# Kernel optimization log

Measured on AMD Instinct MI355X. Metric: run time of the kernel, lower is better.

The kernel has to match this reference:

```python
import jax, jax.numpy as jnp
import numpy as np

# Model constants (match init_kwargs)
NUM_HEADS = 8
IN_BITS = 64
N_STATE = 256
N_OUT = 64
K_CONN = 8            # n_bits_per_output_neuron
HASH = 65536          # hash_size
K_BITS = 3            # routing key bits
B = 128               # batch of independent sequences
T = 128               # timesteps (windows) per sequence


def setup_inputs() -> dict:
    key = jax.random.key(0)
    k1, k2, k3, k4, k5, k6 = jax.random.split(key, 6)
    # flat bit sequences, split into T windows of IN_BITS in reference()
    bits = jax.random.randint(k1, (B, T * IN_BITS), 0, 2, dtype=jnp.int32)
    # state layer: full connectivity (default n_bits_per_state_neuron =
    # input_bits + n_state_neurons), hashed addressing via random odd-ish
    # integer coefficients dotted with the bit vector, mod HASH.
    total_in = IN_BITS + N_STATE  # 320
    state_coeffs = jax.random.randint(k2, (N_STATE, total_in), 1, HASH, dtype=jnp.int32)
    state_mem = jax.random.uniform(k3, (N_STATE, HASH), dtype=jnp.float32)
    # output heads: each neuron connects to K_CONN random state bits
    head_conn = jax.random.randint(k4, (NUM_HEADS, N_OUT, K_CONN), 0, N_STATE, dtype=jnp.int32)
    head_coeffs = jax.random.randint(k5, (NUM_HEADS, N_OUT, K_CONN), 1, HASH, dtype=jnp.int32)
    head_mem = jax.random.uniform(k6, (NUM_HEADS, N_OUT, HASH), dtype=jnp.float32)
    return {
        "bits": bits,
        "state_coeffs": state_coeffs,
        "state_mem": state_mem,
        "head_conn": head_conn,
        "head_coeffs": head_coeffs,
        "head_mem": head_mem,
    }


def reference(bits, state_coeffs, state_mem, head_conn, head_coeffs, head_mem):
    # windows: [B, T, IN_BITS]
    windows = bits.reshape(B, T, IN_BITS)
    n_state, hash_size = state_mem.shape

    def step(state, w):  # state: [B, N_STATE] int32 bits; w: [B, IN_BITS]
        x = jnp.concatenate([w, state], axis=1)                 # [B, IN+N]
        addr = (x @ state_coeffs.T) % hash_size                 # hashed address [B, N]
        vals = state_mem[jnp.arange(n_state), addr]             # gather [B, N]
        new_state = (vals >= 0.5).astype(jnp.int32)             # RAM output bits
        return new_state, None

    state0 = jnp.zeros((B, n_state), jnp.int32)
    final_state, _ = jax.lax.scan(step, state0, jnp.swapaxes(windows, 0, 1))

    # all output heads read the shared final state
    sel = final_state[:, head_conn]                             # [B, H, O, K]
    addr_h = jnp.einsum('bhok,hok->bho', sel, head_coeffs) % hash_size
    head_vals = head_mem[jnp.arange(NUM_HEADS)[:, None],
                         jnp.arange(N_OUT)[None, :], addr_h]    # [B, H, O]

    # kv routing: pack last K_BITS bits of the final window (MSB first)
    last_w = windows[:, -1, :]
    pow2 = 2 ** jnp.arange(K_BITS - 1, -1, -1)
    head_idx = jnp.sum(last_w[:, -K_BITS:] * pow2, axis=1) % NUM_HEADS  # [B]

    out = head_vals[jnp.arange(B), head_idx]                    # [B, N_OUT]
    return out
```

## Files before the change

### kernel.cpp

```cpp
#include <hip/hip_runtime.h>
#include <stdint.h>

#define T_ 128

typedef int v4i __attribute__((ext_vector_type(4)));

__global__ void prep_bfrag(const int* __restrict__ sc, uint4* __restrict__ bf) {
  int gid = blockIdx.x * 256 + threadIdx.x;
  if (gid >= 160 * 64) return;
  int mf = gid >> 6, l = gid & 63;
  int tau = mf / 10, rem = mf % 10;
  int kap = rem >> 1, h = rem & 1;
  int j = 16 * tau + (l & 15);
  int kinb = (l >> 4) * 16;
  unsigned wout[4];
#pragma unroll
  for (int r = 0; r < 4; ++r) {
    unsigned wrd = 0;
#pragma unroll
    for (int be = 0; be < 4; ++be) {
      int kin = kinb + 4 * r + be;
      int col = (kap == 0) ? kin : 64 + ((kap - 1) << 6) + kin;
      unsigned c = (unsigned)sc[j * 320 + col];
      unsigned byte = (h ? (c >> 8) : c) & 0xFFu;
      byte = (byte - 128u) & 0xFFu;
      wrd |= byte << (8 * be);
    }
    wout[r] = wrd;
  }
  bf[gid] = make_uint4(wout[0], wout[1], wout[2], wout[3]);
}

__global__ void prep_wbits(const int* __restrict__ bits,
                           unsigned long long* __restrict__ wb) {
  int gid = blockIdx.x * 256 + threadIdx.x;
  int wv = gid >> 6, lane = gid & 63;
  unsigned long long m = __ballot(bits[gid] != 0);
  if (lane == 0) wb[wv] = m;
}

__global__ void prep_bitpack(const float* __restrict__ sm,
                             unsigned long long* __restrict__ packed) {
  int base = blockIdx.x * (256 * 32) + threadIdx.x;
  int lane = threadIdx.x & 63;
#pragma unroll 1
  for (int it = 0; it < 32; ++it) {
    int idx = base + it * 256;
    float v = sm[idx];
    unsigned long long m = __ballot(v >= 0.5f);
    if (lane == 0) packed[idx >> 6] = m;
  }
}

static __device__ __forceinline__ v4i expand16(unsigned b16) {
  v4i a;
#pragma unroll
  for (int r = 0; r < 4; ++r) {
    unsigned nib = (b16 >> (4 * r)) & 0xFu;
    a[r] = (int)((nib * 0x00204081u) & 0x01010101u);
  }
  return a;
}

__global__ __launch_bounds__(256, 1) void scan_heads(
    const uint4* __restrict__ bfrag,
    const unsigned* __restrict__ packed32,
    const unsigned long long* __restrict__ wbits,
    const int* __restrict__ head_conn,
    const int* __restrict__ head_coeffs,
    const float* __restrict__ head_mem,
    float* __restrict__ out) {
  __shared__ __align__(16) unsigned char ab[2][256];
  __shared__ __align__(16) unsigned mcnt[2][4];
  const int tid = threadIdx.x;
  const int b = blockIdx.x;
  const int w = tid >> 6, l = tid & 63;
  const int qq = l >> 4;
  const int j = 64 * w + l;

  v4i bf[4][5][2];
#pragma unroll
  for (int i = 0; i < 4; ++i)
#pragma unroll
    for (int k = 0; k < 5; ++k)
#pragma unroll
      for (int h = 0; h < 2; ++h) {
        int mf = ((4 * w + i) * 5 + k) * 2 + h;
        bf[i][k][h] = __builtin_bit_cast(v4i, bfrag[mf * 64 + l]);
      }
#pragma unroll
  for (int i = 0; i < 4; ++i)
#pragma unroll
    for (int k = 0; k < 5; ++k)
#pragma unroll
      for (int h = 0; h < 2; ++h)
        asm volatile("" : "+v"(bf[i][k][h]));

  ab[0][tid] = (unsigned char)0;
  if (tid < 4) mcnt[0][tid] = 0u;

  const unsigned* pkrow = packed32 + ((size_t)j << 11);
  unsigned long long wcur = wbits[b * 128];

  v4i wacc[4][2];
  unsigned wcorr;
  {
    v4i aw = expand16((unsigned)((wcur >> (16 * qq)) & 0xFFFFu));
    v4i z = (v4i){0, 0, 0, 0};
#pragma unroll
    for (int i = 0; i < 4; ++i)
#pragma unroll
      for (int h = 0; h < 2; ++h)
        wacc[i][h] = __builtin_amdgcn_mfma_i32_16x16x64_i8(aw, bf[i][0][h], z, 0, 0, 0);
    wcorr = (unsigned)__popcll(wcur) * 32896u;
  }
  __syncthreads();

#pragma unroll 2
  for (int t = 0; t < T_; ++t) {
    const int cur = t & 1, nxt = cur ^ 1;

    int tn = (t + 1 < T_) ? t + 1 : t;
    unsigned long long wnext = wbits[b * 128 + tn];

    const unsigned char* abase = &ab[cur][16 * qq];
    v4i a0 = *(const v4i*)(abase);
    v4i a1 = *(const v4i*)(abase + 64);
    v4i a2 = *(const v4i*)(abase + 128);
    v4i a3 = *(const v4i*)(abase + 192);
    uint4 cz = *((const uint4*)&mcnt[cur][0]);

    v4i z = (v4i){0, 0, 0, 0};
    v4i accP[4][2], accQ[4][2], accR[4][2], accS[4][2];
#pragma unroll
    for (int i = 0; i < 4; ++i) {
      accP[i][0] = __builtin_amdgcn_mfma_i32_16x16x64_i8(a0, bf[i][1][0], wacc[i][0], 0, 0, 0);
      accP[i][1] = __builtin_amdgcn_mfma_i32_16x16x64_i8(a0, bf[i][1][1], wacc[i][1], 0, 0, 0);
      accQ[i][0] = __builtin_amdgcn_mfma_i32_16x16x64_i8(a1, bf[i][2][0], z, 0, 0, 0);
      accQ[i][1] = __builtin_amdgcn_mfma_i32_16x16x64_i8(a1, bf[i][2][1], z, 0, 0, 0);
      accR[i][0] = __builtin_amdgcn_mfma_i32_16x16x64_i8(a2, bf[i][3][0], z, 0, 0, 0);
      accR[i][1] = __builtin_amdgcn_mfma_i32_16x16x64_i8(a2, bf[i][3][1], z, 0, 0, 0);
      accS[i][0] = __builtin_amdgcn_mfma_i32_16x16x64_i8(a3, bf[i][4][0], z, 0, 0, 0);
      accS[i][1] = __builtin_amdgcn_mfma_i32_16x16x64_i8(a3, bf[i][4][1], z, 0, 0, 0);
    }

    unsigned csum = cz.x + cz.y + cz.z + cz.w + wcorr;
    unsigned tv0 = ((unsigned)accP[0][0][0] + (unsigned)accQ[0][0][0] +
                    (unsigned)accR[0][0][0] + (unsigned)accS[0][0][0]) +
                   (((unsigned)accP[0][1][0] + (unsigned)accQ[0][1][0] +
                     (unsigned)accR[0][1][0] + (unsigned)accS[0][1][0]) << 8);
    unsigned tv1 = ((unsigned)accP[1][0][0] + (unsigned)accQ[1][0][0] +
                    (unsigned)accR[1][0][0] + (unsigned)accS[1][0][0]) +
                   (((unsigned)accP[1][1][0] + (unsigned)accQ[1][1][0] +
                     (unsigned)accR[1][1][0] + (unsigned)accS[1][1][0]) << 8);
    unsigned tv2 = ((unsigned)accP[2][0][0] + (unsigned)accQ[2][0][0] +
                    (unsigned)accR[2][0][0] + (unsigned)accS[2][0][0]) +
                   (((unsigned)accP[2][1][0] + (unsigned)accQ[2][1][0] +
                     (unsigned)accR[2][1][0] + (unsigned)accS[2][1][0]) << 8);
    unsigned tv3 = ((unsigned)accP[3][0][0] + (unsigned)accQ[3][0][0] +
                    (unsigned)accR[3][0][0] + (unsigned)accS[3][0][0]) +
                   (((unsigned)accP[3][1][0] + (unsigned)accQ[3][1][0] +
                     (unsigned)accR[3][1][0] + (unsigned)accS[3][1][0]) << 8);
    unsigned t01 = (l & 16) ? tv1 : tv0;
    unsigned t23 = (l & 16) ? tv3 : tv2;
    unsigned ad = (((l & 32) ? t23 : t01) + csum) & 0xFFFFu;

    unsigned word = pkrow[ad >> 5];

    {
      v4i aw = expand16((unsigned)((wnext >> (16 * qq)) & 0xFFFFu));
#pragma unroll
      for (int i = 0; i < 4; ++i)
#pragma unroll
        for (int h = 0; h < 2; ++h)
          wacc[i][h] = __builtin_amdgcn_mfma_i32_16x16x64_i8(aw, bf[i][0][h], z, 0, 0, 0);
      wcorr = (unsigned)__popcll(wnext) * 32896u;
    }

    unsigned bitv = (word >> (ad & 31)) & 1u;
    unsigned long long mq = __ballot(bitv != 0u);
    ab[nxt][j] = (unsigned char)bitv;
    if (l == 0) mcnt[nxt][w] = (unsigned)__popcll(mq) * 32896u;

    asm volatile("s_waitcnt lgkmcnt(0)" ::: "memory");
    __builtin_amdgcn_sched_barrier(0);
    __builtin_amdgcn_s_barrier();
    __builtin_amdgcn_sched_barrier(0);

    wcur = wnext;
  }

  if (w == 0) {
    int h = (int)((((wcur >> 61) & 1) << 2) | (((wcur >> 62) & 1) << 1) |
                  ((wcur >> 63) & 1));
    int ho = h * 64 + l;
    const int4* cn4 = (const int4*)(head_conn + ho * 8);
    const int4* cf4 = (const int4*)(head_coeffs + ho * 8);
    int4 cna = cn4[0], cnb = cn4[1];
    int4 cfa = cf4[0], cfb = cf4[1];
    int cns[8] = {cna.x, cna.y, cna.z, cna.w, cnb.x, cnb.y, cnb.z, cnb.w};
    int cfs[8] = {cfa.x, cfa.y, cfa.z, cfa.w, cfb.x, cfb.y, cfb.z, cfb.w};
    unsigned addr = 0;
#pragma unroll
    for (int k = 0; k < 8; ++k) {
      addr += (unsigned)ab[T_ & 1][cns[k]] * (unsigned)cfs[k];
    }
    addr &= 0xFFFFu;
    out[b * 64 + l] = head_mem[((size_t)ho << 16) + addr];
  }
}

extern "C" void kernel_launch(void* const* d_in, const int* in_sizes, int n_in,
                              void* d_out, int out_size, void* d_ws, size_t ws_size,
                              hipStream_t stream) {
  const int*   bits         = (const int*)d_in[0];
  const int*   state_coeffs = (const int*)d_in[1];
  const float* state_mem    = (const float*)d_in[2];
  const int*   head_conn    = (const int*)d_in[3];
  const int*   head_coeffs  = (const int*)d_in[4];
  const float* head_mem     = (const float*)d_in[5];
  float* out = (float*)d_out;

  char* ws = (char*)d_ws;
  uint4*              bfrag  = (uint4*)ws;
  unsigned long long* wbits  = (unsigned long long*)(ws + (160 << 10));
  unsigned*           packed = (unsigned*)(ws + (288 << 10));

  prep_bfrag<<<40, 256, 0, stream>>>(state_coeffs, bfrag);
  prep_wbits<<<4096, 256, 0, stream>>>(bits, wbits);
  prep_bitpack<<<2048, 256, 0, stream>>>(state_mem, (unsigned long long*)packed);
  scan_heads<<<128, 256, 0, stream>>>(bfrag, packed, wbits,
                                      head_conn, head_coeffs, head_mem, out);
}
```

Measured before the change: 319.4 us.

## Split scan across eight waves with chained MFMA accumulation per wave

Launches the scan kernel with 512 threads so each wave handles 32 state neurons (two 16-column tiles) instead of 64. Each wave now holds half the B-fragments and issues half the MFMAs per step. The four K-chunk MFMAs are chained through one accumulator rather than summed from four separate ones. This shortens the serial per-step critical path, at the cost of half-idle lanes in the gather and ballot and more waves meeting at each barrier.

```diff
diff --git a/kernel.cpp b/kernel.cpp
--- a/kernel.cpp
+++ b/kernel.cpp
@@ -62,7 +62,7 @@
   return a;
 }
 
-__global__ __launch_bounds__(256, 1) void scan_heads(
+__global__ __launch_bounds__(512, 2) void scan_heads(
     const uint4* __restrict__ bfrag,
     const unsigned* __restrict__ packed32,
     const unsigned long long* __restrict__ wbits,
@@ -71,44 +71,37 @@
     const float* __restrict__ head_mem,
     float* __restrict__ out) {
   __shared__ __align__(16) unsigned char ab[2][256];
-  __shared__ __align__(16) unsigned mcnt[2][4];
+  __shared__ __align__(16) unsigned mcnt[2][8];
   const int tid = threadIdx.x;
   const int b = blockIdx.x;
   const int w = tid >> 6, l = tid & 63;
   const int qq = l >> 4;
-  const int j = 64 * w + l;
-
-  v4i bf[4][5][2];
-#pragma unroll
-  for (int i = 0; i < 4; ++i)
+  const int jg = 32 * w + (l & 31);
+
+  v4i bf[2][5][2];
+#pragma unroll
+  for (int i = 0; i < 2; ++i)
 #pragma unroll
     for (int k = 0; k < 5; ++k)
 #pragma unroll
       for (int h = 0; h < 2; ++h) {
-        int mf = ((4 * w + i) * 5 + k) * 2 + h;
+        int mf = ((2 * w + i) * 5 + k) * 2 + h;
         bf[i][k][h] = __builtin_bit_cast(v4i, bfrag[mf * 64 + l]);
       }
-#pragma unroll
-  for (int i = 0; i < 4; ++i)
-#pragma unroll
-    for (int k = 0; k < 5; ++k)
-#pragma unroll
-      for (int h = 0; h < 2; ++h)
-        asm volatile("" : "+v"(bf[i][k][h]));
-
-  ab[0][tid] = (unsigned char)0;
-  if (tid < 4) mcnt[0][tid] = 0u;
-
-  const unsigned* pkrow = packed32 + ((size_t)j << 11);
+
+  if (tid < 256) ab[0][tid] = (unsigned char)0;
+  if (tid < 8) mcnt[0][tid] = 0u;
+
+  const unsigned* pkrow = packed32 + ((size_t)jg << 11);
   unsigned long long wcur = wbits[b * 128];
 
-  v4i wacc[4][2];
+  v4i wacc[2][2];
   unsigned wcorr;
   {
     v4i aw = expand16((unsigned)((wcur >> (16 * qq)) & 0xFFFFu));
     v4i z = (v4i){0, 0, 0, 0};
 #pragma unroll
-    for (int i = 0; i < 4; ++i)
+    for (int i = 0; i < 2; ++i)
 #pragma unroll
       for (int h = 0; h < 2; ++h)
         wacc[i][h] = __builtin_amdgcn_mfma_i32_16x16x64_i8(aw, bf[i][0][h], z, 0, 0, 0);
@@ -128,49 +121,44 @@
     v4i a1 = *(const v4i*)(abase + 64);
     v4i a2 = *(const v4i*)(abase + 128);
     v4i a3 = *(const v4i*)(abase + 192);
-    uint4 cz = *((const uint4*)&mcnt[cur][0]);
-
-    v4i z = (v4i){0, 0, 0, 0};
-    v4i accP[4][2], accQ[4][2], accR[4][2], accS[4][2];
-#pragma unroll
-    for (int i = 0; i < 4; ++i) {
-      accP[i][0] = __builtin_amdgcn_mfma_i32_16x16x64_i8(a0, bf[i][1][0], wacc[i][0], 0, 0, 0);
-      accP[i][1] = __builtin_amdgcn_mfma_i32_16x16x64_i8(a0, bf[i][1][1], wacc[i][1], 0, 0, 0);
-      accQ[i][0] = __builtin_amdgcn_mfma_i32_16x16x64_i8(a1, bf[i][2][0], z, 0, 0, 0);
-      accQ[i][1] = __builtin_amdgcn_mfma_i32_16x16x64_i8(a1, bf[i][2][1], z, 0, 0, 0);
-      accR[i][0] = __builtin_amdgcn_mfma_i32_16x16x64_i8(a2, bf[i][3][0], z, 0, 0, 0);
-      accR[i][1] = __builtin_amdgcn_mfma_i32_16x16x64_i8(a2, bf[i][3][1], z, 0, 0, 0);
-      accS[i][0] = __builtin_amdgcn_mfma_i32_16x16x64_i8(a3, bf[i][4][0], z, 0, 0, 0);
-      accS[i][1] = __builtin_amdgcn_mfma_i32_16x16x64_i8(a3, bf[i][4][1], z, 0, 0, 0);
-    }
-
-    unsigned csum = cz.x + cz.y + cz.z + cz.w + wcorr;
-    unsigned tv0 = ((unsigned)accP[0][0][0] + (unsigned)accQ[0][0][0] +
-                    (unsigned)accR[0][0][0] + (unsigned)accS[0][0][0]) +
-                   (((unsigned)accP[0][1][0] + (unsigned)accQ[0][1][0] +
-                     (unsigned)accR[0][1][0] + (unsigned)accS[0][1][0]) << 8);
-    unsigned tv1 = ((unsigned)accP[1][0][0] + (unsigned)accQ[1][0][0] +
-                    (unsigned)accR[1][0][0] + (unsigned)accS[1][0][0]) +
-                   (((unsigned)accP[1][1][0] + (unsigned)accQ[1][1][0] +
-                     (unsigned)accR[1][1][0] + (unsigned)accS[1][1][0]) << 8);
-    unsigned tv2 = ((unsigned)accP[2][0][0] + (unsigned)accQ[2][0][0] +
-                    (unsigned)accR[2][0][0] + (unsigned)accS[2][0][0]) +
-                   (((unsigned)accP[2][1][0] + (unsigned)accQ[2][1][0] +
-                     (unsigned)accR[2][1][0] + (unsigned)accS[2][1][0]) << 8);
-    unsigned tv3 = ((unsigned)accP[3][0][0] + (unsigned)accQ[3][0][0] +
-                    (unsigned)accR[3][0][0] + (unsigned)accS[3][0][0]) +
-                   (((unsigned)accP[3][1][0] + (unsigned)accQ[3][1][0] +
-                     (unsigned)accR[3][1][0] + (unsigned)accS[3][1][0]) << 8);
-    unsigned t01 = (l & 16) ? tv1 : tv0;
-    unsigned t23 = (l & 16) ? tv3 : tv2;
-    unsigned ad = (((l & 32) ? t23 : t01) + csum) & 0xFFFFu;
-
-    unsigned word = pkrow[ad >> 5];
+    uint4 c0 = *((const uint4*)&mcnt[cur][0]);
+    uint4 c1 = *((const uint4*)&mcnt[cur][4]);
+
+    v4i acc[2][2];
+#pragma unroll
+    for (int i = 0; i < 2; ++i)
+#pragma unroll
+      for (int h = 0; h < 2; ++h)
+        acc[i][h] = __builtin_amdgcn_mfma_i32_16x16x64_i8(a0, bf[i][1][h], wacc[i][h], 0, 0, 0);
+#pragma unroll
+    for (int i = 0; i < 2; ++i)
+#pragma unroll
+      for (int h = 0; h < 2; ++h)
+        acc[i][h] = __builtin_amdgcn_mfma_i32_16x16x64_i8(a1, bf[i][2][h], acc[i][h], 0, 0, 0);
+#pragma unroll
+    for (int i = 0; i < 2; ++i)
+#pragma unroll
+      for (int h = 0; h < 2; ++h)
+        acc[i][h] = __builtin_amdgcn_mfma_i32_16x16x64_i8(a2, bf[i][3][h], acc[i][h], 0, 0, 0);
+#pragma unroll
+    for (int i = 0; i < 2; ++i)
+#pragma unroll
+      for (int h = 0; h < 2; ++h)
+        acc[i][h] = __builtin_amdgcn_mfma_i32_16x16x64_i8(a3, bf[i][4][h], acc[i][h], 0, 0, 0);
+
+    unsigned csum = c0.x + c0.y + c0.z + c0.w + c1.x + c1.y + c1.z + c1.w + wcorr;
+    unsigned tv0 = (unsigned)acc[0][0][0] + ((unsigned)acc[0][1][0] << 8);
+    unsigned tv1 = (unsigned)acc[1][0][0] + ((unsigned)acc[1][1][0] << 8);
+    unsigned ad = (((l & 16) ? tv1 : tv0) + csum) & 0xFFFFu;
+
+    unsigned word = 0;
+    if (l < 32) word = pkrow[ad >> 5];
 
     {
       v4i aw = expand16((unsigned)((wnext >> (16 * qq)) & 0xFFFFu));
-#pragma unroll
-      for (int i = 0; i < 4; ++i)
+      v4i z = (v4i){0, 0, 0, 0};
+#pragma unroll
+      for (int i = 0; i < 2; ++i)
 #pragma unroll
         for (int h = 0; h < 2; ++h)
           wacc[i][h] = __builtin_amdgcn_mfma_i32_16x16x64_i8(aw, bf[i][0][h], z, 0, 0, 0);
@@ -178,9 +166,9 @@
     }
 
     unsigned bitv = (word >> (ad & 31)) & 1u;
-    unsigned long long mq = __ballot(bitv != 0u);
-    ab[nxt][j] = (unsigned char)bitv;
-    if (l == 0) mcnt[nxt][w] = (unsigned)__popcll(mq) * 32896u;
+    unsigned long long mq = __ballot(l < 32 && bitv != 0u);
+    if (l < 32) ab[nxt][jg] = (unsigned char)bitv;
+    if (l == 0) mcnt[nxt][w] = (unsigned)__popc((unsigned)mq) * 32896u;
 
     asm volatile("s_waitcnt lgkmcnt(0)" ::: "memory");
     __builtin_amdgcn_sched_barrier(0);
@@ -229,6 +217,6 @@
   prep_bfrag<<<40, 256, 0, stream>>>(state_coeffs, bfrag);
   prep_wbits<<<4096, 256, 0, stream>>>(bits, wbits);
   prep_bitpack<<<2048, 256, 0, stream>>>(state_mem, (unsigned long long*)packed);
-  scan_heads<<<128, 256, 0, stream>>>(bfrag, packed, wbits,
+  scan_heads<<<128, 512, 0, stream>>>(bfrag, packed, wbits,
                                       head_conn, head_coeffs, head_mem, out);
 }
```

Result: no change. 314.0 us (-1.7%).

## Pack two sequences per block and replace s_barrier with per-group LDS counter spin

Applied to the files above, without the earlier changes.

Each block now processes two batch rows with four waves each, halving the grid to 64 blocks of 512 threads. The per-timestep workgroup barrier is replaced by an LDS atomic counter per group, and each wave spin-waits until all four waves of its group have arrived. This lets the two groups proceed independently and avoids full-block barrier cost. The risks are spin-loop overhead and the missing explicit lgkmcnt wait before the arrival signal. Removing the asm register pins and raising the launch bounds also changes register pressure and occupancy.

```diff
diff --git a/kernel.cpp b/kernel.cpp
--- a/kernel.cpp
+++ b/kernel.cpp
@@ -62,7 +62,7 @@
   return a;
 }
 
-__global__ __launch_bounds__(256, 1) void scan_heads(
+__global__ __launch_bounds__(512, 2) void scan_heads(
     const uint4* __restrict__ bfrag,
     const unsigned* __restrict__ packed32,
     const unsigned long long* __restrict__ wbits,
@@ -70,13 +70,15 @@
     const int* __restrict__ head_coeffs,
     const float* __restrict__ head_mem,
     float* __restrict__ out) {
-  __shared__ __align__(16) unsigned char ab[2][256];
-  __shared__ __align__(16) unsigned mcnt[2][4];
+  __shared__ __align__(16) unsigned char ab[2][2][256];
+  __shared__ __align__(16) unsigned mcnt[2][2][4];
+  __shared__ unsigned ctr[2];
   const int tid = threadIdx.x;
-  const int b = blockIdx.x;
   const int w = tid >> 6, l = tid & 63;
+  const int g = w >> 2, wg = w & 3;
   const int qq = l >> 4;
-  const int j = 64 * w + l;
+  const int j = 64 * wg + l;
+  const int row = 2 * blockIdx.x + g;
 
   v4i bf[4][5][2];
 #pragma unroll
@@ -85,22 +87,16 @@
     for (int k = 0; k < 5; ++k)
 #pragma unroll
       for (int h = 0; h < 2; ++h) {
-        int mf = ((4 * w + i) * 5 + k) * 2 + h;
+        int mf = ((4 * wg + i) * 5 + k) * 2 + h;
         bf[i][k][h] = __builtin_bit_cast(v4i, bfrag[mf * 64 + l]);
       }
-#pragma unroll
-  for (int i = 0; i < 4; ++i)
-#pragma unroll
-    for (int k = 0; k < 5; ++k)
-#pragma unroll
-      for (int h = 0; h < 2; ++h)
-        asm volatile("" : "+v"(bf[i][k][h]));
-
-  ab[0][tid] = (unsigned char)0;
-  if (tid < 4) mcnt[0][tid] = 0u;
+
+  ab[g][0][tid & 255] = (unsigned char)0;
+  if ((tid & 255) < 4) mcnt[g][0][tid & 255] = 0u;
+  if ((tid & 255) == 0) ctr[g] = 0u;
 
   const unsigned* pkrow = packed32 + ((size_t)j << 11);
-  unsigned long long wcur = wbits[b * 128];
+  unsigned long long wcur = wbits[row * 128];
 
   v4i wacc[4][2];
   unsigned wcorr;
@@ -121,14 +117,14 @@
     const int cur = t & 1, nxt = cur ^ 1;
 
     int tn = (t + 1 < T_) ? t + 1 : t;
-    unsigned long long wnext = wbits[b * 128 + tn];
-
-    const unsigned char* abase = &ab[cur][16 * qq];
+    unsigned long long wnext = wbits[row * 128 + tn];
+
+    const unsigned char* abase = &ab[g][cur][16 * qq];
     v4i a0 = *(const v4i*)(abase);
     v4i a1 = *(const v4i*)(abase + 64);
     v4i a2 = *(const v4i*)(abase + 128);
     v4i a3 = *(const v4i*)(abase + 192);
-    uint4 cz = *((const uint4*)&mcnt[cur][0]);
+    uint4 cz = *((const uint4*)&mcnt[g][cur][0]);
 
     v4i z = (v4i){0, 0, 0, 0};
     v4i accP[4][2], accQ[4][2], accR[4][2], accS[4][2];
@@ -179,18 +175,22 @@
 
     unsigned bitv = (word >> (ad & 31)) & 1u;
     unsigned long long mq = __ballot(bitv != 0u);
-    ab[nxt][j] = (unsigned char)bitv;
-    if (l == 0) mcnt[nxt][w] = (unsigned)__popcll(mq) * 32896u;
-
-    asm volatile("s_waitcnt lgkmcnt(0)" ::: "memory");
+    ab[g][nxt][j] = (unsigned char)bitv;
+    if (l == 0) mcnt[g][nxt][wg] = (unsigned)__popcll(mq) * 32896u;
+
+    if (l == 0)
+      __hip_atomic_fetch_add(&ctr[g], 1u, __ATOMIC_RELEASE,
+                             __HIP_MEMORY_SCOPE_WORKGROUP);
+    const unsigned tgt = 4u * (unsigned)(t + 1);
+    while (__hip_atomic_load(&ctr[g], __ATOMIC_ACQUIRE,
+                             __HIP_MEMORY_SCOPE_WORKGROUP) < tgt) {
+    }
     __builtin_amdgcn_sched_barrier(0);
-    __builtin_amdgcn_s_barrier();
-    __builtin_amdgcn_sched_barrier(0);
 
     wcur = wnext;
   }
 
-  if (w == 0) {
+  if (wg == 0) {
     int h = (int)((((wcur >> 61) & 1) << 2) | (((wcur >> 62) & 1) << 1) |
                   ((wcur >> 63) & 1));
     int ho = h * 64 + l;
@@ -203,10 +203,10 @@
     unsigned addr = 0;
 #pragma unroll
     for (int k = 0; k < 8; ++k) {
-      addr += (unsigned)ab[T_ & 1][cns[k]] * (unsigned)cfs[k];
+      addr += (unsigned)ab[g][T_ & 1][cns[k]] * (unsigned)cfs[k];
     }
     addr &= 0xFFFFu;
-    out[b * 64 + l] = head_mem[((size_t)ho << 16) + addr];
+    out[row * 64 + l] = head_mem[((size_t)ho << 16) + addr];
   }
 }
 
@@ -229,6 +229,6 @@
   prep_bfrag<<<40, 256, 0, stream>>>(state_coeffs, bfrag);
   prep_wbits<<<4096, 256, 0, stream>>>(bits, wbits);
   prep_bitpack<<<2048, 256, 0, stream>>>(state_mem, (unsigned long long*)packed);
-  scan_heads<<<128, 256, 0, stream>>>(bfrag, packed, wbits,
-                                      head_conn, head_coeffs, head_mem, out);
-}
+  scan_heads<<<64, 512, 0, stream>>>(bfrag, packed, wbits,
+                                     head_conn, head_coeffs, head_mem, out);
+}
```

Measured after the change: 371.5 us. 16.3% more time.
